# Kernel optimization log

Hardware: AMD Instinct MI355X
Metric: run time of the kernel (lower is better)

The kernel has to match this reference:

```python
import jax, jax.numpy as jnp
import numpy as np

N_HEADS = 8; N_LEVELS = 4; T_WINDOW = 2; N_CURR = 4; N_TEMP = 2; D_MODEL = 256
D_HEAD = D_MODEL // N_HEADS
SHAPES = [[4, 32, 48], [4, 16, 24], [4, 8, 12], [4, 4, 6]]  # (T, H, W) per level
LEN_IN = sum(t * h * w for t, h, w in SHAPES)  # 8160
LEN_Q = LEN_IN
N_BATCH = 1


def _bilinear_sample(value_l, loc):
    # value_l: (N, M, H, W, D); loc: (N, M, Q, P, 2) normalized to [0, 1].
    # Matches torch grid_sample(mode='bilinear', padding_mode='zeros', align_corners=False)
    # with grid = 2*loc - 1, i.e. pixel coords x = loc_x*W - 0.5, y = loc_y*H - 0.5.
    N, M, H, W, D = value_l.shape
    Q, P = loc.shape[2], loc.shape[3]
    x = loc[..., 0] * W - 0.5
    y = loc[..., 1] * H - 0.5
    x0 = jnp.floor(x); y0 = jnp.floor(y)
    wx = x - x0; wy = y - y0
    flat = value_l.reshape(N, M, H * W, D)

    def gather(xi, yi):
        valid = ((xi >= 0) & (xi < W) & (yi >= 0) & (yi < H)).astype(value_l.dtype)
        idx = (jnp.clip(yi, 0, H - 1) * W + jnp.clip(xi, 0, W - 1)).astype(jnp.int32)
        g = jnp.take_along_axis(flat, idx.reshape(N, M, Q * P, 1), axis=2)
        return g.reshape(N, M, Q, P, D) * valid[..., None]

    v00 = gather(x0, y0); v10 = gather(x0 + 1.0, y0)
    v01 = gather(x0, y0 + 1.0); v11 = gather(x0 + 1.0, y0 + 1.0)
    return (v00 * ((1 - wx) * (1 - wy))[..., None] + v10 * (wx * (1 - wy))[..., None]
            + v01 * ((1 - wx) * wy)[..., None] + v11 * (wx * wy)[..., None])


def _forward(query, reference_points, temporal_offsets, input_flatten, shapes, starts,
             Wv, bv, Ws, bs, Wa, ba, Wts, bts, Wta, bta, Wo, bo):
    N, Lq, _ = query.shape
    value = (input_flatten @ Wv + bv).reshape(N, -1, N_HEADS, D_HEAD)
    ts_off = (query @ Wts + bts).reshape(N, Lq, N_HEADS, N_LEVELS, T_WINDOW, N_TEMP, 2)
    t_attn = (query @ Wta + bta).reshape(N, Lq, N_HEADS, N_LEVELS * T_WINDOW * N_TEMP)
    c_attn = (query @ Wa + ba).reshape(N, Lq, N_HEADS, N_LEVELS * N_CURR)
    # joint softmax over current + temporal sampling points (as in the source)
    attn = jax.nn.softmax(jnp.concatenate([c_attn, t_attn], axis=-1), axis=-1)
    aw_c = attn[..., :N_LEVELS * N_CURR].reshape(N, Lq, N_HEADS, N_LEVELS, N_CURR)
    aw_t = attn[..., N_LEVELS * N_CURR:].reshape(N, Lq, N_HEADS, N_LEVELS, T_WINDOW * N_TEMP)
    aw = jnp.concatenate([aw_c, aw_t], axis=4)  # (N, Lq, M, L, P)
    c_off = (query @ Ws + bs).reshape(N, Lq, N_HEADS, N_LEVELS, N_CURR, 2)
    # flattened-temporal grid per level: width W_l, height T_l*H_l
    norm = jnp.array([[w, t * h] for t, h, w in shapes], dtype=query.dtype)  # (L, 2)
    loc_c = reference_points[:, :, None, :, None, :] + c_off / norm[None, None, None, :, None, :]
    loc_t = (reference_points[:, :, None, :, None, None, :]
             + temporal_offsets[:, :, None, :, :, None, :]
             + ts_off / norm[None, None, None, :, None, None, :])
    loc_t = loc_t.reshape(N, Lq, N_HEADS, N_LEVELS, T_WINDOW * N_TEMP, 2)
    locs = jnp.concatenate([loc_c, loc_t], axis=4)  # (N, Lq, M, L, P, 2)
    out = jnp.zeros((N, N_HEADS, Lq, D_HEAD), query.dtype)
    for l, (t, h, w) in enumerate(shapes):
        s = starts[l]
        vl = value[:, s:s + t * h * w].transpose(0, 2, 1, 3).reshape(N, N_HEADS, t * h, w, D_HEAD)
        loc_l = locs[:, :, :, l].transpose(0, 2, 1, 3, 4)   # (N, M, Lq, P, 2)
        sampled = _bilinear_sample(vl, loc_l)               # (N, M, Lq, P, Dh)
        w_l = aw[:, :, :, l].transpose(0, 2, 1, 3)          # (N, M, Lq, P)
        out = out + jnp.einsum('nmqpd,nmqp->nmqd', sampled, w_l)
    out = out.transpose(0, 2, 1, 3).reshape(N, Lq, D_MODEL)
    return out @ Wo + bo


def setup_inputs() -> dict:
    key = jax.random.key(0)
    ks = jax.random.split(key, 18)
    D = D_MODEL
    sc = 0.02
    query = jax.random.normal(ks[0], (N_BATCH, LEN_Q, D), jnp.float32)
    reference_points = jax.random.uniform(ks[1], (N_BATCH, LEN_Q, N_LEVELS, 2), jnp.float32)
    temporal_offsets = jax.random.uniform(ks[2], (N_BATCH, LEN_Q, N_LEVELS, T_WINDOW, 2),
                                          jnp.float32, minval=-0.25, maxval=0.25)
    input_flatten = jax.random.normal(ks[3], (N_BATCH, LEN_IN, D), jnp.float32)
    input_spatial_shapes = jnp.array(SHAPES, dtype=jnp.int32)
    starts = np.cumsum([0] + [t * h * w for t, h, w in SHAPES])[:-1]
    input_level_start_index = jnp.array(starts, dtype=jnp.int32)
    n_off = N_HEADS * N_LEVELS * N_CURR * 2          # 256
    n_att = N_HEADS * N_LEVELS * N_CURR              # 128
    n_toff = N_HEADS * N_LEVELS * T_WINDOW * N_TEMP * 2  # 256
    n_tatt = N_HEADS * N_LEVELS * T_WINDOW * N_TEMP      # 128
    return {
        'query': query, 'reference_points': reference_points,
        'temporal_offsets': temporal_offsets, 'input_flatten': input_flatten,
        'input_spatial_shapes': input_spatial_shapes,
        'input_level_start_index': input_level_start_index,
        'Wv': jax.random.normal(ks[4], (D, D), jnp.float32) * sc,
        'bv': jnp.zeros((D,), jnp.float32),
        'Ws': jax.random.normal(ks[5], (D, n_off), jnp.float32) * sc,
        'bs': jax.random.normal(ks[6], (n_off,), jnp.float32) * 2.0,
        'Wa': jax.random.normal(ks[7], (D, n_att), jnp.float32) * sc,
        'ba': jnp.zeros((n_att,), jnp.float32),
        'Wts': jax.random.normal(ks[8], (D, n_toff), jnp.float32) * sc,
        'bts': jax.random.normal(ks[9], (n_toff,), jnp.float32) * 2.0,
        'Wta': jax.random.normal(ks[10], (D, n_tatt), jnp.float32) * sc,
        'bta': jnp.zeros((n_tatt,), jnp.float32),
        'Wo': jax.random.normal(ks[11], (D, D), jnp.float32) * sc,
        'bo': jnp.zeros((D,), jnp.float32),
    }


def reference(query, reference_points, temporal_offsets, input_flatten,
              input_spatial_shapes, input_level_start_index,
              Wv, bv, Ws, bs, Wa, ba, Wts, bts, Wta, bta, Wo, bo):
    shapes = [tuple(int(v) for v in row) for row in np.asarray(input_spatial_shapes)]
    starts = [int(v) for v in np.asarray(input_level_start_index)]
    return _forward(query, reference_points, temporal_offsets, input_flatten,
                    shapes, starts, Wv, bv, Ws, bs, Wa, ba, Wts, bts, Wta, bta, Wo, bo)
```

## Files before the change

### kernel.cpp

```cpp
#include <hip/hip_runtime.h>


#define LEN 8160
#define NPACK8 (1280 * 256 / 8)

typedef __attribute__((ext_vector_type(8))) short bf16x8;
typedef __attribute__((ext_vector_type(8))) unsigned short u16x8;
typedef __attribute__((ext_vector_type(4))) float f32x4;

__device__ __forceinline__ unsigned short rne_bf16(float v)
{
    unsigned u = __float_as_uint(v);
    return (unsigned short)((u + 0x7FFFu + ((u >> 16) & 1u)) >> 16);
}

__device__ __forceinline__ void split_bf16(float v, unsigned short* hi, unsigned short* lo)
{
    unsigned u = __float_as_uint(v);
    unsigned r = (u + 0x7FFFu + ((u >> 16) & 1u)) & 0xFFFF0000u;
    float hif = __uint_as_float(r);
    float lof = v - hif;
    unsigned ul = __float_as_uint(lof);
    unsigned rl = (ul + 0x7FFFu + ((ul >> 16) & 1u)) >> 16;
    *hi = (unsigned short)(r >> 16);
    *lo = (unsigned short)rl;
}

__device__ __forceinline__ float bf2f(unsigned short s)
{
    return __uint_as_float(((unsigned)s) << 16);
}

__device__ __forceinline__ void splitA8(const float* a, bf16x8* hi, bf16x8* lo)
{
    float4 x = *(const float4*)a;
    float4 y = *(const float4*)(a + 4);
    unsigned short h[8], l[8];
    split_bf16(x.x, &h[0], &l[0]); split_bf16(x.y, &h[1], &l[1]);
    split_bf16(x.z, &h[2], &l[2]); split_bf16(x.w, &h[3], &l[3]);
    split_bf16(y.x, &h[4], &l[4]); split_bf16(y.y, &h[5], &l[5]);
    split_bf16(y.z, &h[6], &l[6]); split_bf16(y.w, &h[7], &l[7]);
    bf16x8 hv, lv;
    #pragma unroll
    for (int i = 0; i < 8; i++) { hv[i] = (short)h[i]; lv[i] = (short)l[i]; }
    *hi = hv; *lo = lv;
}

__global__ __launch_bounds__(256) void prep_kernel(
    const float* __restrict__ Ws, const float* __restrict__ bs,
    const float* __restrict__ Wa, const float* __restrict__ ba,
    const float* __restrict__ Wts, const float* __restrict__ bts,
    const float* __restrict__ Wta, const float* __restrict__ bta,
    const float* __restrict__ Wv, const float* __restrict__ Wo,
    unsigned short* __restrict__ Whi, unsigned short* __restrict__ Wlo,
    float* __restrict__ bcat)
{
    int idx = blockIdx.x * 256 + threadIdx.x;
    if (idx < NPACK8) {
        int n = idx >> 5;
        int k0 = (idx & 31) << 3;
        unsigned short h[8], l[8];
        #pragma unroll
        for (int t = 0; t < 8; t++) {
            int k = k0 + t;
            float v;
            if (n < 256) v = Wv[k * 256 + n];
            else if (n < 1024) {
                int j = n - 256;
                if (j < 256)      v = Ws [k * 256 + j];
                else if (j < 384) v = Wa [k * 128 + (j - 256)];
                else if (j < 640) v = Wts[k * 256 + (j - 384)];
                else              v = Wta[k * 128 + (j - 640)];
            } else v = Wo[k * 256 + (n - 1024)];
            split_bf16(v, &h[t], &l[t]);
        }
        uint4 hv, lv;
        hv.x = h[0] | ((unsigned)h[1] << 16); hv.y = h[2] | ((unsigned)h[3] << 16);
        hv.z = h[4] | ((unsigned)h[5] << 16); hv.w = h[6] | ((unsigned)h[7] << 16);
        lv.x = l[0] | ((unsigned)l[1] << 16); lv.y = l[2] | ((unsigned)l[3] << 16);
        lv.z = l[4] | ((unsigned)l[5] << 16); lv.w = l[6] | ((unsigned)l[7] << 16);
        *(uint4*)(Whi + n * 256 + k0) = hv;
        *(uint4*)(Wlo + n * 256 + k0) = lv;
    } else if (idx < NPACK8 + 768) {
        int j = idx - NPACK8;
        float v;
        if (j < 256)      v = bs[j];
        else if (j < 384) v = ba[j - 256];
        else if (j < 640) v = bts[j - 384];
        else              v = bta[j - 640];
        bcat[j] = v;
    }
}

__global__ __launch_bounds__(256) void gemm_mfma_dual(
    const float* __restrict__ A0,
    const unsigned short* __restrict__ B0hi, const unsigned short* __restrict__ B0lo,
    const float* __restrict__ bias0, void* __restrict__ C0, int N0, int mode0, int nbx0,
    const float* __restrict__ A1,
    const unsigned short* __restrict__ B1hi, const unsigned short* __restrict__ B1lo,
    const float* __restrict__ bias1, void* __restrict__ C1, int N1, int mode1)
{
    __shared__ unsigned short Bf[2 * 4 * 4 * 64 * 8];
    const int tid = threadIdx.x;
    const int wave = tid >> 6, lane = tid & 63;
    int bx = blockIdx.x;
    const int by = blockIdx.y;

    const float* A;
    const unsigned short *Bhi, *Blo;
    const float* bias; void* C; int N, mode;
    if (bx < nbx0) {
        A = A0; Bhi = B0hi; Blo = B0lo;
        bias = bias0; C = C0; N = N0; mode = mode0;
    } else {
        bx -= nbx0;
        A = A1; Bhi = B1hi; Blo = B1lo;
        bias = bias1; C = C1; N = N1; mode = mode1;
    }

    const int lm = lane & 15;
    const int kq = lane >> 4;
    const int m0 = by * 128 + wave * 32 + lm;
    const int ra = min(m0, LEN - 1);
    const int rb = min(m0 + 16, LEN - 1);
    const float* aP0 = A + (size_t)ra * 256 + kq * 8;
    const float* aP1 = A + (size_t)rb * 256 + kq * 8;

    f32x4 acc[2][4] = {};
    #pragma unroll
    for (int chunk = 0; chunk < 2; chunk++) {
        #pragma unroll
        for (int t = 0; t < 8; t++) {
            int f = t * 256 + tid;
            int ln = f & 63, nt = (f >> 6) & 3, kt = (f >> 8) & 3, pl = f >> 10;
            const unsigned short* src = (pl ? Blo : Bhi)
                + (size_t)(bx * 64 + nt * 16 + (ln & 15)) * 256
                + chunk * 128 + kt * 32 + (ln >> 4) * 8;
            *(uint4*)(&Bf[(size_t)f * 8]) = *(const uint4*)src;
        }
        __syncthreads();
        #pragma unroll
        for (int kt = 0; kt < 4; kt++) {
            const int ko = chunk * 128 + kt * 32;
            bf16x8 ah0, al0, ah1, al1;
            splitA8(aP0 + ko, &ah0, &al0);
            splitA8(aP1 + ko, &ah1, &al1);
            #pragma unroll
            for (int nt = 0; nt < 4; nt++) {
                const int fb = (kt * 4 + nt) * 64 + lane;
                bf16x8 bh = *(const bf16x8*)(&Bf[(size_t)fb * 8]);
                bf16x8 bl = *(const bf16x8*)(&Bf[(size_t)(fb + 1024) * 8]);
                acc[0][nt] = __builtin_amdgcn_mfma_f32_16x16x32_bf16(ah0, bh, acc[0][nt], 0, 0, 0);
                acc[0][nt] = __builtin_amdgcn_mfma_f32_16x16x32_bf16(ah0, bl, acc[0][nt], 0, 0, 0);
                acc[0][nt] = __builtin_amdgcn_mfma_f32_16x16x32_bf16(al0, bh, acc[0][nt], 0, 0, 0);
                acc[1][nt] = __builtin_amdgcn_mfma_f32_16x16x32_bf16(ah1, bh, acc[1][nt], 0, 0, 0);
                acc[1][nt] = __builtin_amdgcn_mfma_f32_16x16x32_bf16(ah1, bl, acc[1][nt], 0, 0, 0);
                acc[1][nt] = __builtin_amdgcn_mfma_f32_16x16x32_bf16(al1, bh, acc[1][nt], 0, 0, 0);
            }
        }
        __syncthreads();
    }

    const int col = bx * 64 + lm;
    #pragma unroll
    for (int sub = 0; sub < 2; sub++) {
        const int row0 = by * 128 + wave * 32 + sub * 16 + kq * 4;
        #pragma unroll
        for (int nt = 0; nt < 4; nt++) {
            int c = col + nt * 16;
            float bb = bias[c];
            #pragma unroll
            for (int r = 0; r < 4; r++) {
                int row = row0 + r;
                if (row < LEN) {
                    float v = acc[sub][nt][r] + bb;
                    if (mode) {
                        ((unsigned short*)C)[(size_t)(c >> 5) * 8192 * 32
                                             + (size_t)row * 32 + (c & 31)] = rne_bf16(v);
                    } else {
                        ((float*)C)[(size_t)row * N + c] = v;
                    }
                }
            }
        }
    }
}

__global__ __launch_bounds__(256) void sample_kernel(
    const unsigned short* __restrict__ value,
    const float* __restrict__ proj,
    const float* __restrict__ refp,
    const float* __restrict__ toff,
    float* __restrict__ attn)
{
    const int q = blockIdx.x;
    const int head = threadIdx.x >> 5;
    const int lane = threadIdx.x & 31;
    __shared__ int2   s_row[8][32];
    __shared__ float4 s_w[8][32];

    const float* p = proj + (size_t)q * 768;

    {
        const int i = lane;
        float logit, ox, oy, rx, ry;
        int l;
        if (i < 16) {
            l = i >> 2; int pt2 = i & 3;
            logit = p[256 + head * 16 + i];
            ox = p[head * 32 + l * 8 + pt2 * 2 + 0];
            oy = p[head * 32 + l * 8 + pt2 * 2 + 1];
            rx = refp[q * 8 + l * 2 + 0];
            ry = refp[q * 8 + l * 2 + 1];
        } else {
            int j = i - 16; l = j >> 2;
            int tp = j & 3, tw = tp >> 1, nt = tp & 1;
            logit = p[640 + head * 16 + j];
            ox = p[384 + head * 32 + l * 8 + tw * 4 + nt * 2 + 0];
            oy = p[384 + head * 32 + l * 8 + tw * 4 + nt * 2 + 1];
            rx = refp[q * 8 + l * 2 + 0] + toff[q * 16 + l * 4 + tw * 2 + 0];
            ry = refp[q * 8 + l * 2 + 1] + toff[q * 16 + l * 4 + tw * 2 + 1];
        }
        const int Wl = 48 >> l;
        const int Hgl = 128 >> l;
        const int st = 8192 - (8192 >> (2 * l));
        const float fW = (float)Wl, fHg = (float)Hgl;
        float x = (rx + ox / fW) * fW - 0.5f;
        float y = (ry + oy / fHg) * fHg - 0.5f;

        float mx = logit;
        #pragma unroll
        for (int off = 16; off > 0; off >>= 1)
            mx = fmaxf(mx, __shfl_xor(mx, off, 32));
        float e = expf(logit - mx);
        float s = e;
        #pragma unroll
        for (int off = 16; off > 0; off >>= 1)
            s += __shfl_xor(s, off, 32);
        float w = e / s;

        float fx = floorf(x), fy = floorf(y);
        float wx = x - fx, wy = y - fy;
        int x0 = (int)fx, y0 = (int)fy;
        int x1 = x0 + 1, y1 = y0 + 1;
        float mx0 = ((unsigned)x0 < (unsigned)Wl) ? 1.f : 0.f;
        float mx1 = ((unsigned)x1 < (unsigned)Wl) ? 1.f : 0.f;
        float my0 = ((unsigned)y0 < (unsigned)Hgl) ? 1.f : 0.f;
        float my1 = ((unsigned)y1 < (unsigned)Hgl) ? 1.f : 0.f;
        int cx0 = min(max(x0, 0), Wl - 1), cx1 = min(max(x1, 0), Wl - 1);
        int cy0 = min(max(y0, 0), Hgl - 1), cy1 = min(max(y1, 0), Hgl - 1);
        int xb = min(max(x0, 0), Wl - 2);
        float sx0 = 1.f - wx, sy0 = 1.f - wy;
        float aL = (cx0 == xb     ? sx0 * mx0 : 0.f) + (cx1 == xb     ? wx * mx1 : 0.f);
        float aR = (cx0 == xb + 1 ? sx0 * mx0 : 0.f) + (cx1 == xb + 1 ? wx * mx1 : 0.f);
        float by0 = sy0 * my0, by1 = wy * my1;
        int2 rr;
        rr.x = (st + cy0 * Wl + xb) * 64;
        rr.y = (st + cy1 * Wl + xb) * 64;
        float4 ww;
        ww.x = w * aL * by0;
        ww.y = w * aR * by0;
        ww.z = w * aL * by1;
        ww.w = w * aR * by1;
        s_row[head][lane] = rr;
        s_w[head][lane] = ww;
    }
    __syncthreads();

    const int pt4  = lane >> 3;
    const int half = (lane >> 2) & 1;
    const int cg   = lane & 3;
    const char* vbase = (const char*)value + head * (8192 * 64) + half * 64 + cg * 16;
    float acc[8] = {0.f, 0.f, 0.f, 0.f, 0.f, 0.f, 0.f, 0.f};
    #pragma unroll
    for (int i = 0; i < 8; i++) {
        int pidx = (i << 2) | pt4;
        int2 rr = s_row[head][pidx];
        float4 ww = s_w[head][pidx];
        u16x8 v0 = *(const u16x8*)(vbase + rr.x);
        u16x8 v1 = *(const u16x8*)(vbase + rr.y);
        float w0 = half ? ww.y : ww.x;
        float w1 = half ? ww.w : ww.z;
        #pragma unroll
        for (int j = 0; j < 8; j++) {
            acc[j] = fmaf(w0, bf2f(v0[j]), acc[j]);
            acc[j] = fmaf(w1, bf2f(v1[j]), acc[j]);
        }
    }
    #pragma unroll
    for (int off = 4; off <= 16; off <<= 1)
        #pragma unroll
        for (int j = 0; j < 8; j++)
            acc[j] += __shfl_xor(acc[j], off, 32);

    if (lane < 4) {
        size_t o = (size_t)q * 256 + head * 32 + cg * 8;
        *(float4*)(attn + o)     = make_float4(acc[0], acc[1], acc[2], acc[3]);
        *(float4*)(attn + o + 4) = make_float4(acc[4], acc[5], acc[6], acc[7]);
    }
}

extern "C" void kernel_launch(void* const* d_in, const int* in_sizes, int n_in,
                              void* d_out, int out_size, void* d_ws, size_t ws_size,
                              hipStream_t stream)
{
    const float* query = (const float*)d_in[0];
    const float* refp  = (const float*)d_in[1];
    const float* toff  = (const float*)d_in[2];
    const float* inpf  = (const float*)d_in[3];
    const float* Wv  = (const float*)d_in[6];
    const float* bv  = (const float*)d_in[7];
    const float* Ws_ = (const float*)d_in[8];
    const float* bs_ = (const float*)d_in[9];
    const float* Wa  = (const float*)d_in[10];
    const float* ba  = (const float*)d_in[11];
    const float* Wts = (const float*)d_in[12];
    const float* bts = (const float*)d_in[13];
    const float* Wta = (const float*)d_in[14];
    const float* bta = (const float*)d_in[15];
    const float* Wo  = (const float*)d_in[16];
    const float* bo  = (const float*)d_in[17];
    float* out = (float*)d_out;

    unsigned short* value_bf = (unsigned short*)d_ws;
    float* proj = (float*)(value_bf + (size_t)8 * 8192 * 32);
    float* attn = proj + (size_t)LEN * 768;
    unsigned short* Whi = (unsigned short*)(attn + (size_t)LEN * 256);
    unsigned short* Wlo = Whi + 1280 * 256;
    float* bcat = (float*)(Wlo + 1280 * 256);

    prep_kernel<<<164, 256, 0, stream>>>(Ws_, bs_, Wa, ba, Wts, bts, Wta, bta,
                                         Wv, Wo, Whi, Wlo, bcat);
    gemm_mfma_dual<<<dim3(16, 64), 256, 0, stream>>>(
        inpf, Whi, Wlo, bv, value_bf, 256, 1, 4,
        query, Whi + 256 * 256, Wlo + 256 * 256, bcat, proj, 768, 0);
    sample_kernel<<<LEN, 256, 0, stream>>>(value_bf, proj, refp, toff, attn);
    gemm_mfma_dual<<<dim3(4, 64), 256, 0, stream>>>(
        attn, Whi + 1024 * 256, Wlo + 1024 * 256, bo, out, 256, 0, 4,
        attn, Whi + 1024 * 256, Wlo + 1024 * 256, bo, out, 256, 0);
}
```

Measured before the change: 173.9 us.

## Truncate A split in GEMM, pack sampler FMAs, two queries per block

The GEMM A-operand split now truncates the high bf16 half instead of rounding it, and packs halves with bit operations, cutting ALU work in the inner loop. The sampler accumulates with 2-wide float vectors so the compiler can emit packed FMAs, and it converts bf16 to float with shift and mask. Each sampler block now processes two queries with 512 threads, halving the number of blocks. Truncating the high half changes how the error is split between the hi and lo parts, which may slightly alter precision.

After: 178.4 us. +2.6%, slower.

```diff
diff --git a/kernel.cpp b/kernel.cpp
--- a/kernel.cpp
+++ b/kernel.cpp
@@ -5,8 +5,8 @@
 #define NPACK8 (1280 * 256 / 8)
 
 typedef __attribute__((ext_vector_type(8))) short bf16x8;
-typedef __attribute__((ext_vector_type(8))) unsigned short u16x8;
 typedef __attribute__((ext_vector_type(4))) float f32x4;
+typedef __attribute__((ext_vector_type(2))) float f32x2;
 
 __device__ __forceinline__ unsigned short rne_bf16(float v)
 {
@@ -26,24 +26,25 @@
     *lo = (unsigned short)rl;
 }
 
-__device__ __forceinline__ float bf2f(unsigned short s)
-{
-    return __uint_as_float(((unsigned)s) << 16);
-}
-
-__device__ __forceinline__ void splitA8(const float* a, bf16x8* hi, bf16x8* lo)
-{
-    float4 x = *(const float4*)a;
-    float4 y = *(const float4*)(a + 4);
-    unsigned short h[8], l[8];
-    split_bf16(x.x, &h[0], &l[0]); split_bf16(x.y, &h[1], &l[1]);
-    split_bf16(x.z, &h[2], &l[2]); split_bf16(x.w, &h[3], &l[3]);
-    split_bf16(y.x, &h[4], &l[4]); split_bf16(y.y, &h[5], &l[5]);
-    split_bf16(y.z, &h[6], &l[6]); split_bf16(y.w, &h[7], &l[7]);
-    bf16x8 hv, lv;
-    #pragma unroll
-    for (int i = 0; i < 8; i++) { hv[i] = (short)h[i]; lv[i] = (short)l[i]; }
-    *hi = hv; *lo = lv;
+__device__ __forceinline__ void splitA8f(const float* a, bf16x8* hi, bf16x8* lo)
+{
+    uint4 ua = *(const uint4*)a;
+    uint4 ub = *(const uint4*)(a + 4);
+    unsigned u[8] = {ua.x, ua.y, ua.z, ua.w, ub.x, ub.y, ub.z, ub.w};
+    unsigned hp[4], lp[4];
+    #pragma unroll
+    for (int t = 0; t < 4; t++) {
+        unsigned h0 = u[2 * t] & 0xFFFF0000u;
+        unsigned h1 = u[2 * t + 1] & 0xFFFF0000u;
+        float l0 = __uint_as_float(u[2 * t])     - __uint_as_float(h0);
+        float l1 = __uint_as_float(u[2 * t + 1]) - __uint_as_float(h1);
+        hp[t] = (u[2 * t] >> 16) | h1;
+        lp[t] = (__float_as_uint(l0) >> 16) | (__float_as_uint(l1) & 0xFFFF0000u);
+    }
+    uint4 hv = make_uint4(hp[0], hp[1], hp[2], hp[3]);
+    uint4 lv = make_uint4(lp[0], lp[1], lp[2], lp[3]);
+    *hi = *(bf16x8*)&hv;
+    *lo = *(bf16x8*)&lv;
 }
 
 __global__ __launch_bounds__(256) void prep_kernel(
@@ -143,8 +144,8 @@
         for (int kt = 0; kt < 4; kt++) {
             const int ko = chunk * 128 + kt * 32;
             bf16x8 ah0, al0, ah1, al1;
-            splitA8(aP0 + ko, &ah0, &al0);
-            splitA8(aP1 + ko, &ah1, &al1);
+            splitA8f(aP0 + ko, &ah0, &al0);
+            splitA8f(aP1 + ko, &ah1, &al1);
             #pragma unroll
             for (int nt = 0; nt < 4; nt++) {
                 const int fb = (kt * 4 + nt) * 64 + lane;
@@ -186,18 +187,20 @@
     }
 }
 
-__global__ __launch_bounds__(256) void sample_kernel(
+__global__ __launch_bounds__(512) void sample_kernel(
     const unsigned short* __restrict__ value,
     const float* __restrict__ proj,
     const float* __restrict__ refp,
     const float* __restrict__ toff,
     float* __restrict__ attn)
 {
-    const int q = blockIdx.x;
-    const int head = threadIdx.x >> 5;
-    const int lane = threadIdx.x & 31;
-    __shared__ int2   s_row[8][32];
-    __shared__ float4 s_w[8][32];
+    const int sub  = threadIdx.x >> 8;
+    const int t2   = threadIdx.x & 255;
+    const int head = t2 >> 5;
+    const int lane = t2 & 31;
+    const int q = blockIdx.x * 2 + sub;
+    __shared__ int2   s_row[2][8][32];
+    __shared__ float4 s_w[2][8][32];
 
     const float* p = proj + (size_t)q * 768;
 
@@ -262,8 +265,8 @@
         ww.y = w * aR * by0;
         ww.z = w * aL * by1;
         ww.w = w * aR * by1;
-        s_row[head][lane] = rr;
-        s_w[head][lane] = ww;
+        s_row[sub][head][lane] = rr;
+        s_w[sub][head][lane] = ww;
     }
     __syncthreads();
 
@@ -271,22 +274,32 @@
     const int half = (lane >> 2) & 1;
     const int cg   = lane & 3;
     const char* vbase = (const char*)value + head * (8192 * 64) + half * 64 + cg * 16;
-    float acc[8] = {0.f, 0.f, 0.f, 0.f, 0.f, 0.f, 0.f, 0.f};
+    f32x2 acc2[4] = {};
     #pragma unroll
     for (int i = 0; i < 8; i++) {
         int pidx = (i << 2) | pt4;
-        int2 rr = s_row[head][pidx];
-        float4 ww = s_w[head][pidx];
-        u16x8 v0 = *(const u16x8*)(vbase + rr.x);
-        u16x8 v1 = *(const u16x8*)(vbase + rr.y);
+        int2 rr = s_row[sub][head][pidx];
+        float4 ww = s_w[sub][head][pidx];
+        uint4 v0 = *(const uint4*)(vbase + rr.x);
+        uint4 v1 = *(const uint4*)(vbase + rr.y);
         float w0 = half ? ww.y : ww.x;
         float w1 = half ? ww.w : ww.z;
-        #pragma unroll
-        for (int j = 0; j < 8; j++) {
-            acc[j] = fmaf(w0, bf2f(v0[j]), acc[j]);
-            acc[j] = fmaf(w1, bf2f(v1[j]), acc[j]);
-        }
-    }
+        f32x2 w0v = {w0, w0}, w1v = {w1, w1};
+        unsigned d0[4] = {v0.x, v0.y, v0.z, v0.w};
+        unsigned d1[4] = {v1.x, v1.y, v1.z, v1.w};
+        #pragma unroll
+        for (int t = 0; t < 4; t++) {
+            f32x2 c0 = { __uint_as_float(d0[t] << 16),
+                         __uint_as_float(d0[t] & 0xFFFF0000u) };
+            f32x2 c1 = { __uint_as_float(d1[t] << 16),
+                         __uint_as_float(d1[t] & 0xFFFF0000u) };
+            acc2[t] = w0v * c0 + acc2[t];
+            acc2[t] = w1v * c1 + acc2[t];
+        }
+    }
+    float acc[8];
+    #pragma unroll
+    for (int t = 0; t < 4; t++) { acc[2 * t] = acc2[t].x; acc[2 * t + 1] = acc2[t].y; }
     #pragma unroll
     for (int off = 4; off <= 16; off <<= 1)
         #pragma unroll
@@ -334,7 +347,7 @@
     gemm_mfma_dual<<<dim3(16, 64), 256, 0, stream>>>(
         inpf, Whi, Wlo, bv, value_bf, 256, 1, 4,
         query, Whi + 256 * 256, Wlo + 256 * 256, bcat, proj, 768, 0);
-    sample_kernel<<<LEN, 256, 0, stream>>>(value_bf, proj, refp, toff, attn);
+    sample_kernel<<<LEN / 2, 512, 0, stream>>>(value_bf, proj, refp, toff, attn);
     gemm_mfma_dual<<<dim3(4, 64), 256, 0, stream>>>(
         attn, Whi + 1024 * 256, Wlo + 1024 * 256, bo, out, 256, 0, 4,
         attn, Whi + 1024 * 256, Wlo + 1024 * 256, bo, out, 256, 0);
```
